# Kernel tuning notes

Hardware: AMD Instinct MI355X
Metric: run time of the kernel (lower is better)

Reference implementation:

```python
import jax, jax.numpy as jnp
import numpy as np

B = 32768
D_IN = 512
UNITS = 512


def setup_inputs() -> dict:
    key = jax.random.key(0)
    ks = jax.random.split(key, 12)
    s = 1.0 / np.sqrt(D_IN)
    sh = 1.0 / np.sqrt(UNITS)
    return {
        "inputs": jax.random.normal(ks[0], (B, D_IN), dtype=jnp.float32),
        "state": jax.random.normal(ks[1], (B, UNITS), dtype=jnp.float32),
        "att_score": jax.random.uniform(ks[2], (B, 1), dtype=jnp.float32),
        # update gate
        "Wu_x": jax.random.normal(ks[3], (D_IN, UNITS), dtype=jnp.float32) * s,
        "bu": jnp.zeros((UNITS,), dtype=jnp.float32),
        "Wu_h": jax.random.normal(ks[4], (UNITS, UNITS), dtype=jnp.float32) * sh,
        # reset gate
        "Wr_x": jax.random.normal(ks[5], (D_IN, UNITS), dtype=jnp.float32) * s,
        "br": jnp.zeros((UNITS,), dtype=jnp.float32),
        "Wr_h": jax.random.normal(ks[6], (UNITS, UNITS), dtype=jnp.float32) * sh,
        # candidate memory
        "Wc_x": jax.random.normal(ks[7], (D_IN, UNITS), dtype=jnp.float32) * s,
        "bc": jnp.zeros((UNITS,), dtype=jnp.float32),
        "Wc_h": jax.random.normal(ks[8], (UNITS, UNITS), dtype=jnp.float32) * sh,
    }


def reference(inputs, state, att_score, Wu_x, bu, Wu_h, Wr_x, br, Wr_h, Wc_x, bc, Wc_h):
    # u = sigmoid(Dense_act(x) + Dense_noact(h))
    u = jax.nn.sigmoid(inputs @ Wu_x + bu + state @ Wu_h)
    # r = sigmoid(Dense_act(x) + Dense_noact(h))
    r = jax.nn.sigmoid(inputs @ Wr_x + br + state @ Wr_h)
    # c = tanh(Dense_act(x) + r * Dense_noact(h))
    c = jnp.tanh(inputs @ Wc_x + bc + r * (state @ Wc_h))
    u_ = att_score * u  # [B,1] * [B,U] broadcast
    state_next = (1.0 - u_) * state + u_ * c
    return state_next
```

## Files before the change

### kernel.cpp

```cpp
#include <hip/hip_runtime.h>
#include <hip/hip_bf16.h>
#include <stdint.h>

#define B_ROWS 32768
#define DIM 512
#define THREADS 256
#define NKT 32
#define ABUF 8192
#define WBUF 12288
#define BUF (ABUF + WBUF)

typedef __attribute__((ext_vector_type(8))) __bf16 bf16x8;
typedef __attribute__((ext_vector_type(4))) float f32x4;
typedef __attribute__((ext_vector_type(4))) unsigned int uint4v;

__device__ static inline unsigned short f2bf(float f) {
    unsigned int u = __builtin_bit_cast(unsigned int, f);
    u += 0x7fffu + ((u >> 16) & 1u);
    return (unsigned short)(u >> 16);
}

__device__ static inline void load_lds_16B(const void* g, void* lds) {
    __builtin_amdgcn_global_load_lds(
        (const __attribute__((address_space(1))) unsigned int*)g,
        (__attribute__((address_space(3))) unsigned int*)lds,
        16, 0, 0);
}

__global__ void prep_weights(const float* __restrict__ Wu_x, const float* __restrict__ Wu_h,
                             const float* __restrict__ Wr_x, const float* __restrict__ Wr_h,
                             const float* __restrict__ Wc_x, const float* __restrict__ Wc_h,
                             unsigned short* __restrict__ Wt2) {
    __shared__ float tile[32][33];
    const int t = blockIdx.z;
    const int k0 = blockIdx.x * 32;
    const int n0 = blockIdx.y * 32;
    const float* Wx = (t == 0) ? Wu_x : (t == 1) ? Wr_x : Wc_x;
    const float* Wh = (t == 0) ? Wu_h : (t == 1) ? Wr_h : Wc_h;
    const int tid = threadIdx.x;
    const int c = tid & 31, r0 = tid >> 5;
#pragma unroll
    for (int i = 0; i < 4; ++i) {
        int kl = r0 + i * 8;
        int k = k0 + kl;
        int n = n0 + c;
        float v = (k < 512) ? Wx[(size_t)k * 512 + n] : Wh[(size_t)(k - 512) * 512 + n];
        tile[kl][c] = v;
    }
    __syncthreads();
    const int kt = k0 >> 5;
#pragma unroll
    for (int i = 0; i < 4; ++i) {
        int nl = r0 + i * 8;
        int kc = c;
        int n = n0 + nl;
        size_t base = (((size_t)kt * 3 + t) * 512 + n) * 64;
        *(unsigned short*)((char*)Wt2 + base + ((kc * 2) ^ (((n >> 1) & 3) << 4))) =
            f2bf(tile[kc][nl]);
    }
}

__global__ __launch_bounds__(512) void prep_A(const float* __restrict__ x,
                                              const float* __restrict__ h,
                                              unsigned short* __restrict__ Apack) {
    const size_t i = (size_t)blockIdx.x * 512 + threadIdx.x;
    const int slot = (int)(i & 3);
    const int row = (int)((i >> 2) & 32767);
    const int kt = (int)(i >> 17);
    const int k0 = kt * 32 + slot * 8;
    const float* src = (k0 < 512) ? (x + (size_t)row * 512 + k0)
                                  : (h + (size_t)row * 512 + (k0 - 512));
    float4 f0 = *(const float4*)(src + 0);
    float4 f1 = *(const float4*)(src + 4);
    uint4v p;
    p.x = f2bf(f0.x) | ((unsigned)f2bf(f0.y) << 16);
    p.y = f2bf(f0.z) | ((unsigned)f2bf(f0.w) << 16);
    p.z = f2bf(f1.x) | ((unsigned)f2bf(f1.y) << 16);
    p.w = f2bf(f1.z) | ((unsigned)f2bf(f1.w) << 16);
    char* dst = (char*)Apack + (((size_t)kt << 15) + row) * 64
              + ((slot * 16) ^ (((row >> 1) & 3) << 4));
    *(uint4v*)dst = p;
}

__global__ __launch_bounds__(THREADS, 2) void augru_main(
    const float* __restrict__ h, const float* __restrict__ att,
    const unsigned short* __restrict__ Wt2, const unsigned short* __restrict__ Apack,
    const float* __restrict__ bu, const float* __restrict__ br,
    const float* __restrict__ bc, float* __restrict__ out) {
    extern __shared__ char smem[];
    const int tid = threadIdx.x;
    const int lane = tid & 63;
    const int wid = tid >> 6;
    const int wm = wid >> 1;
    const int wn = wid & 1;
    const int id = blockIdx.x;
    const int wg = (id & 7) * 256 + (id >> 3);
    const int nb = wg & 7;
    const int mb = wg >> 3;
    const int cl = lane & 15;
    const int kg = lane >> 4;

    f32x4 accU[4][2], accR[4][2], accCx[4][2], accCh[4][2];
#pragma unroll
    for (int i = 0; i < 4; ++i)
#pragma unroll
        for (int j = 0; j < 2; ++j) {
            accU[i][j] = (f32x4)(0.f);
            accR[i][j] = (f32x4)(0.f);
            accCx[i][j] = (f32x4)(0.f);
            accCh[i][j] = (f32x4)(0.f);
        }

    int aOff[4], wOff[3][2];
#pragma unroll
    for (int mi = 0; mi < 4; ++mi) {
        const int row = wm * 64 + mi * 16 + cl;
        aOff[mi] = row * 64 + ((kg * 16) ^ (((row >> 1) & 3) << 4));
    }
#pragma unroll
    for (int t = 0; t < 3; ++t)
#pragma unroll
        for (int ni = 0; ni < 2; ++ni) {
            const int col = wn * 32 + ni * 16 + cl;
            wOff[t][ni] = ABUF + t * 4096 + col * 64
                        + ((kg * 16) ^ (((col >> 1) & 3) << 4));
        }

    const char* gA0 = (const char*)Apack + ((size_t)mb * 128) * 64 + tid * 16;
    const char* gW0 = (const char*)Wt2 + ((size_t)nb * 64) * 64 + tid * 16;

    auto stage = [&](int buf, int kt) {
        char* base = smem + buf * BUF;
        const char* gA = gA0 + (size_t)kt * (32768 * 64);
        const char* gW = gW0 + (size_t)kt * (3 * 512 * 64);
        load_lds_16B(gA, base + wid * 1024);
        load_lds_16B(gA + 4096, base + 4096 + wid * 1024);
#pragma unroll
        for (int t = 0; t < 3; ++t)
            load_lds_16B(gW + (size_t)t * (512 * 64),
                         base + ABUF + t * 4096 + wid * 1024);
    };

    stage(0, 0);
    stage(1, 1);
    stage(2, 2);

    auto body = [&](int kt, int buf, int wait, f32x4(&accC)[4][2]) {
        if (wait == 10)     asm volatile("s_waitcnt vmcnt(10)" ::: "memory");
        else if (wait == 5) asm volatile("s_waitcnt vmcnt(5)" ::: "memory");
        else                asm volatile("s_waitcnt vmcnt(0)" ::: "memory");
        __builtin_amdgcn_s_barrier();
        if (kt + 3 < NKT) stage((kt + 3) & 3, kt + 3);
        const char* aB = smem + buf * BUF;
        bf16x8 a[4], bb[3][2];
#pragma unroll
        for (int mi = 0; mi < 4; ++mi)
            a[mi] = __builtin_bit_cast(bf16x8, *(const uint4v*)(aB + aOff[mi]));
#pragma unroll
        for (int t = 0; t < 3; ++t)
#pragma unroll
            for (int ni = 0; ni < 2; ++ni)
                bb[t][ni] = __builtin_bit_cast(bf16x8,
                    *(const uint4v*)(aB + wOff[t][ni]));
        __builtin_amdgcn_s_setprio(1);
#pragma unroll
        for (int ni = 0; ni < 2; ++ni) {
#pragma unroll
            for (int mi = 0; mi < 4; ++mi)
                accU[mi][ni] = __builtin_amdgcn_mfma_f32_16x16x32_bf16(
                    a[mi], bb[0][ni], accU[mi][ni], 0, 0, 0);
#pragma unroll
            for (int mi = 0; mi < 4; ++mi)
                accR[mi][ni] = __builtin_amdgcn_mfma_f32_16x16x32_bf16(
                    a[mi], bb[1][ni], accR[mi][ni], 0, 0, 0);
#pragma unroll
            for (int mi = 0; mi < 4; ++mi)
                accC[mi][ni] = __builtin_amdgcn_mfma_f32_16x16x32_bf16(
                    a[mi], bb[2][ni], accC[mi][ni], 0, 0, 0);
        }
        __builtin_amdgcn_s_setprio(0);
    };

    for (int g = 0; g < 4; ++g) {
        const int k0 = g * 4;
        body(k0 + 0, 0, 10, accCx);
        body(k0 + 1, 1, 10, accCx);
        body(k0 + 2, 2, 10, accCx);
        body(k0 + 3, 3, 10, accCx);
    }
    for (int g = 4; g < 7; ++g) {
        const int k0 = g * 4;
        body(k0 + 0, 0, 10, accCh);
        body(k0 + 1, 1, 10, accCh);
        body(k0 + 2, 2, 10, accCh);
        body(k0 + 3, 3, 10, accCh);
    }
    body(28, 0, 10, accCh);
    body(29, 1, 10, accCh);
    body(30, 2, 5, accCh);
    body(31, 3, 0, accCh);

#pragma unroll
    for (int ni = 0; ni < 2; ++ni) {
        const int col = nb * 64 + wn * 32 + ni * 16 + cl;
        const float bU = bu[col];
        const float bR = br[col];
        const float bC = bc[col];
#pragma unroll
        for (int mi = 0; mi < 4; ++mi) {
#pragma unroll
            for (int j = 0; j < 4; ++j) {
                const int row = mb * 128 + wm * 64 + mi * 16 + kg * 4 + j;
                const float up = accU[mi][ni][j] + bU;
                const float rp = accR[mi][ni][j] + bR;
                const float u = 1.f / (1.f + __expf(-up));
                const float r = 1.f / (1.f + __expf(-rp));
                const float cpre = accCx[mi][ni][j] + bC + r * accCh[mi][ni][j];
                const float e = __expf(-2.f * cpre);
                const float cc = (1.f - e) / (1.f + e);
                const float aa = att[row];
                const float hv = h[(size_t)row * 512 + col];
                const float u_ = aa * u;
                out[(size_t)row * 512 + col] = (1.f - u_) * hv + u_ * cc;
            }
        }
    }
}

extern "C" void kernel_launch(void* const* d_in, const int* in_sizes, int n_in,
                              void* d_out, int out_size, void* d_ws, size_t ws_size,
                              hipStream_t stream) {
    const float* x    = (const float*)d_in[0];
    const float* h    = (const float*)d_in[1];
    const float* att  = (const float*)d_in[2];
    const float* Wu_x = (const float*)d_in[3];
    const float* bu   = (const float*)d_in[4];
    const float* Wu_h = (const float*)d_in[5];
    const float* Wr_x = (const float*)d_in[6];
    const float* br   = (const float*)d_in[7];
    const float* Wr_h = (const float*)d_in[8];
    const float* Wc_x = (const float*)d_in[9];
    const float* bc   = (const float*)d_in[10];
    const float* Wc_h = (const float*)d_in[11];
    unsigned short* Wt2 = (unsigned short*)d_ws;
    unsigned short* Apack = (unsigned short*)((char*)d_ws + (4 << 20));
    float* out = (float*)d_out;

    prep_weights<<<dim3(32, 16, 3), 256, 0, stream>>>(Wu_x, Wu_h, Wr_x, Wr_h, Wc_x, Wc_h, Wt2);
    prep_A<<<dim3(8192), 512, 0, stream>>>(x, h, Apack);

    hipFuncSetAttribute((const void*)augru_main,
                        hipFuncAttributeMaxDynamicSharedMemorySize, 4 * BUF);
    augru_main<<<dim3(2048), THREADS, 4 * BUF, stream>>>(
        h, att, Wt2, Apack, bu, br, bc, out);
}
```

Before: 147.3 us.

## Fuse activation bf16 conversion into main GEMM kernel, drop prep_A pass

Removes the separate prep_A kernel that converted x and h to a packed, swizzled bf16 buffer. The main kernel now loads fp32 activation rows into registers one k-step ahead, converts them with v_cvt_pk_bf16_f32, and writes them to LDS, while weights keep using async LDS loads. This aims to eliminate the extra global write and re-read of the packed activation buffer and one kernel launch. The cost is twice the activation bytes per block read from cache, plus extra VALU and register work inside the pipelined loop.

```diff
diff --git a/kernel.cpp b/kernel.cpp
--- a/kernel.cpp
+++ b/kernel.cpp
@@ -60,31 +60,9 @@
     }
 }
 
-__global__ __launch_bounds__(512) void prep_A(const float* __restrict__ x,
-                                              const float* __restrict__ h,
-                                              unsigned short* __restrict__ Apack) {
-    const size_t i = (size_t)blockIdx.x * 512 + threadIdx.x;
-    const int slot = (int)(i & 3);
-    const int row = (int)((i >> 2) & 32767);
-    const int kt = (int)(i >> 17);
-    const int k0 = kt * 32 + slot * 8;
-    const float* src = (k0 < 512) ? (x + (size_t)row * 512 + k0)
-                                  : (h + (size_t)row * 512 + (k0 - 512));
-    float4 f0 = *(const float4*)(src + 0);
-    float4 f1 = *(const float4*)(src + 4);
-    uint4v p;
-    p.x = f2bf(f0.x) | ((unsigned)f2bf(f0.y) << 16);
-    p.y = f2bf(f0.z) | ((unsigned)f2bf(f0.w) << 16);
-    p.z = f2bf(f1.x) | ((unsigned)f2bf(f1.y) << 16);
-    p.w = f2bf(f1.z) | ((unsigned)f2bf(f1.w) << 16);
-    char* dst = (char*)Apack + (((size_t)kt << 15) + row) * 64
-              + ((slot * 16) ^ (((row >> 1) & 3) << 4));
-    *(uint4v*)dst = p;
-}
-
 __global__ __launch_bounds__(THREADS, 2) void augru_main(
-    const float* __restrict__ h, const float* __restrict__ att,
-    const unsigned short* __restrict__ Wt2, const unsigned short* __restrict__ Apack,
+    const float* __restrict__ x, const float* __restrict__ h,
+    const float* __restrict__ att, const unsigned short* __restrict__ Wt2,
     const float* __restrict__ bu, const float* __restrict__ br,
     const float* __restrict__ bc, float* __restrict__ out) {
     extern __shared__ char smem[];
@@ -111,57 +89,87 @@
             accCh[i][j] = (f32x4)(0.f);
         }
 
-    int aOff[4], wOff[3][2];
-#pragma unroll
-    for (int mi = 0; mi < 4; ++mi) {
-        const int row = wm * 64 + mi * 16 + cl;
-        aOff[mi] = row * 64 + ((kg * 16) ^ (((row >> 1) & 3) << 4));
-    }
-#pragma unroll
-    for (int t = 0; t < 3; ++t)
-#pragma unroll
-        for (int ni = 0; ni < 2; ++ni) {
-            const int col = wn * 32 + ni * 16 + cl;
-            wOff[t][ni] = ABUF + t * 4096 + col * 64
-                        + ((kg * 16) ^ (((col >> 1) & 3) << 4));
-        }
-
-    const char* gA0 = (const char*)Apack + ((size_t)mb * 128) * 64 + tid * 16;
+    const int rowb = wm * 64 + cl;
+    const int aBase = rowb * 64 + ((kg * 16) ^ (((rowb >> 1) & 3) << 4));
+    const int colb = wn * 32 + cl;
+    const int wBase = ABUF + colb * 64 + ((kg * 16) ^ (((colb >> 1) & 3) << 4));
+
+    const int arow = tid >> 1;
+    const int ap = tid & 1;
+    const int asw = ((arow >> 1) & 3) << 4;
+    const int dsA0 = arow * 64 + ((ap * 32) ^ asw);
+    const int dsA1 = arow * 64 + ((ap * 32 + 16) ^ asw);
+    const float* pAx = x + (size_t)(mb * 128 + arow) * 512 + ap * 16;
+    const float* pAh = h + (size_t)(mb * 128 + arow) * 512 - 512 + ap * 16;
+
     const char* gW0 = (const char*)Wt2 + ((size_t)nb * 64) * 64 + tid * 16;
-
-    auto stage = [&](int buf, int kt) {
+    auto stageW = [&](int buf, int kt) {
         char* base = smem + buf * BUF;
-        const char* gA = gA0 + (size_t)kt * (32768 * 64);
         const char* gW = gW0 + (size_t)kt * (3 * 512 * 64);
-        load_lds_16B(gA, base + wid * 1024);
-        load_lds_16B(gA + 4096, base + 4096 + wid * 1024);
 #pragma unroll
         for (int t = 0; t < 3; ++t)
             load_lds_16B(gW + (size_t)t * (512 * 64),
                          base + ABUF + t * 4096 + wid * 1024);
     };
 
-    stage(0, 0);
-    stage(1, 1);
-    stage(2, 2);
-
-    auto body = [&](int kt, int buf, int wait, f32x4(&accC)[4][2]) {
-        if (wait == 10)     asm volatile("s_waitcnt vmcnt(10)" ::: "memory");
-        else if (wait == 5) asm volatile("s_waitcnt vmcnt(5)" ::: "memory");
-        else                asm volatile("s_waitcnt vmcnt(0)" ::: "memory");
+    f32x4 fa0, fa1, fa2, fa3;
+    auto issueA = [&](int ktn) {
+        const float* g = ((ktn < 16) ? pAx : pAh) + ktn * 32;
+        asm volatile(
+            "global_load_dwordx4 %0, %4, off\n\t"
+            "global_load_dwordx4 %1, %4, off offset:16\n\t"
+            "global_load_dwordx4 %2, %4, off offset:32\n\t"
+            "global_load_dwordx4 %3, %4, off offset:48"
+            : "=&v"(fa0), "=&v"(fa1), "=&v"(fa2), "=&v"(fa3)
+            : "v"(g)
+            : "memory");
+    };
+
+    auto cvt2 = [](float lo, float hi) {
+        unsigned int r;
+        asm("v_cvt_pk_bf16_f32 %0, %1, %2" : "=v"(r) : "v"(lo), "v"(hi));
+        return r;
+    };
+
+    auto convertA = [&](int bufA, bool wLive) {
+        if (wLive) asm volatile("s_waitcnt vmcnt(3)" ::: "memory");
+        else       asm volatile("s_waitcnt vmcnt(0)" ::: "memory");
+        __builtin_amdgcn_sched_barrier(0);
+        uint4v q0, q1;
+        q0.x = cvt2(fa0[0], fa0[1]); q0.y = cvt2(fa0[2], fa0[3]);
+        q0.z = cvt2(fa1[0], fa1[1]); q0.w = cvt2(fa1[2], fa1[3]);
+        q1.x = cvt2(fa2[0], fa2[1]); q1.y = cvt2(fa2[2], fa2[3]);
+        q1.z = cvt2(fa3[0], fa3[1]); q1.w = cvt2(fa3[2], fa3[3]);
+        char* base = smem + bufA * BUF;
+        *(uint4v*)(base + dsA0) = q0;
+        *(uint4v*)(base + dsA1) = q1;
+    };
+
+    stageW(0, 0);
+    stageW(1, 1);
+    stageW(2, 2);
+    issueA(0);
+    convertA(0, false);
+
+    auto body = [&](int kt, int buf, int bufA, f32x4(&accC)[4][2]) {
+        asm volatile("s_waitcnt lgkmcnt(0)" ::: "memory");
         __builtin_amdgcn_s_barrier();
-        if (kt + 3 < NKT) stage((kt + 3) & 3, kt + 3);
+        const bool doA = (kt + 1 < NKT);
+        const bool doW = (kt + 3 < NKT);
+        if (doA) issueA(kt + 1);
+        if (doW) stageW((kt + 3) & 3, kt + 3);
         const char* aB = smem + buf * BUF;
         bf16x8 a[4], bb[3][2];
 #pragma unroll
         for (int mi = 0; mi < 4; ++mi)
-            a[mi] = __builtin_bit_cast(bf16x8, *(const uint4v*)(aB + aOff[mi]));
+            a[mi] = __builtin_bit_cast(bf16x8,
+                *(const uint4v*)(aB + aBase + mi * 1024));
 #pragma unroll
         for (int t = 0; t < 3; ++t)
 #pragma unroll
             for (int ni = 0; ni < 2; ++ni)
                 bb[t][ni] = __builtin_bit_cast(bf16x8,
-                    *(const uint4v*)(aB + wOff[t][ni]));
+                    *(const uint4v*)(aB + wBase + t * 4096 + ni * 1024));
         __builtin_amdgcn_s_setprio(1);
 #pragma unroll
         for (int ni = 0; ni < 2; ++ni) {
@@ -179,26 +187,23 @@
                     a[mi], bb[2][ni], accC[mi][ni], 0, 0, 0);
         }
         __builtin_amdgcn_s_setprio(0);
+        if (doA) convertA(bufA, doW);
     };
 
     for (int g = 0; g < 4; ++g) {
         const int k0 = g * 4;
-        body(k0 + 0, 0, 10, accCx);
-        body(k0 + 1, 1, 10, accCx);
-        body(k0 + 2, 2, 10, accCx);
-        body(k0 + 3, 3, 10, accCx);
-    }
-    for (int g = 4; g < 7; ++g) {
+        body(k0 + 0, 0, 1, accCx);
+        body(k0 + 1, 1, 2, accCx);
+        body(k0 + 2, 2, 3, accCx);
+        body(k0 + 3, 3, 0, accCx);
+    }
+    for (int g = 4; g < 8; ++g) {
         const int k0 = g * 4;
-        body(k0 + 0, 0, 10, accCh);
-        body(k0 + 1, 1, 10, accCh);
-        body(k0 + 2, 2, 10, accCh);
-        body(k0 + 3, 3, 10, accCh);
-    }
-    body(28, 0, 10, accCh);
-    body(29, 1, 10, accCh);
-    body(30, 2, 5, accCh);
-    body(31, 3, 0, accCh);
+        body(k0 + 0, 0, 1, accCh);
+        body(k0 + 1, 1, 2, accCh);
+        body(k0 + 2, 2, 3, accCh);
+        body(k0 + 3, 3, 0, accCh);
+    }
 
 #pragma unroll
     for (int ni = 0; ni < 2; ++ni) {
@@ -243,14 +248,12 @@
     const float* bc   = (const float*)d_in[10];
     const float* Wc_h = (const float*)d_in[11];
     unsigned short* Wt2 = (unsigned short*)d_ws;
-    unsigned short* Apack = (unsigned short*)((char*)d_ws + (4 << 20));
     float* out = (float*)d_out;
 
     prep_weights<<<dim3(32, 16, 3), 256, 0, stream>>>(Wu_x, Wu_h, Wr_x, Wr_h, Wc_x, Wc_h, Wt2);
-    prep_A<<<dim3(8192), 512, 0, stream>>>(x, h, Apack);
 
     hipFuncSetAttribute((const void*)augru_main,
                         hipFuncAttributeMaxDynamicSharedMemorySize, 4 * BUF);
     augru_main<<<dim3(2048), THREADS, 4 * BUF, stream>>>(
-        h, att, Wt2, Apack, bu, br, bc, out);
-}
+        x, h, att, Wt2, bu, br, bc, out);
+}
```

Result: faster. 139.0 us (-5.6%).
